# Kernel optimization log

Measured on AMD Instinct MI355X. Metric: run time of the kernel, lower is better.

The kernel has to match this reference:

```python
import jax, jax.numpy as jnp
import numpy as np

B, S, D, H = 2, 2048, 1024, 16
HD = D // H  # head dim = 64


def setup_inputs() -> dict:
    key = jax.random.key(0)
    ks = jax.random.split(key, 8)
    s = 0.02
    return {
        "Q": jax.random.normal(ks[0], (B, S, D), jnp.float32),
        "K": jax.random.normal(ks[1], (B, S, D), jnp.float32),
        "V": jax.random.normal(ks[2], (B, S, D), jnp.float32),
        "mask": jax.random.randint(ks[3], (1, 1, S, S), 0, 2, jnp.int32),
        "Wq": jax.random.normal(ks[4], (D, D), jnp.float32) * s,
        "bq": jnp.zeros((D,), jnp.float32),
        "Wk": jax.random.normal(ks[5], (D, D), jnp.float32) * s,
        "bk": jnp.zeros((D,), jnp.float32),
        "Wv": jax.random.normal(ks[6], (D, D), jnp.float32) * s,
        "bv": jnp.zeros((D,), jnp.float32),
        "Wo": jax.random.normal(ks[7], (D, D), jnp.float32) * s,
        "bo": jnp.zeros((D,), jnp.float32),
    }


def reference(Q, K, V, mask, Wq, bq, Wk, bk, Wv, bv, Wo, bo):
    b = Q.shape[0]
    # QKV projections, split into heads: [B,S,D] -> [B,H,S,HD]
    q = (Q @ Wq + bq).reshape(b, -1, H, HD).transpose(0, 2, 1, 3)
    k = (K @ Wk + bk).reshape(b, -1, H, HD).transpose(0, 2, 1, 3)
    v = (V @ Wv + bv).reshape(b, -1, H, HD).transpose(0, 2, 1, 3)
    # scaled dot-product attention with full [B,H,S,S] scores (as in source)
    scale = jnp.sqrt(jnp.asarray(HD, q.dtype))
    scores = jnp.einsum("bhqd,bhkd->bhqk", q, k) / scale
    scores = jnp.where(mask == 0, -jnp.inf, scores)
    attn = jax.nn.softmax(scores, axis=-1)
    ctx = jnp.einsum("bhqk,bhkd->bhqd", attn, v)
    # merge heads and output projection
    concat = ctx.transpose(0, 2, 1, 3).reshape(b, -1, H * HD)
    return concat @ Wo + bo
```

## Files before the change

kernel.cpp:

```cpp
#include <hip/hip_runtime.h>


using s8v = __attribute__((ext_vector_type(8))) short;
using f4v = __attribute__((ext_vector_type(4))) float;

__device__ __forceinline__ unsigned short f2bf(float f) {
  union { float f; unsigned int u; } v; v.f = f;
  return (unsigned short)((v.u + 0x7fffu + ((v.u >> 16) & 1u)) >> 16);
}

__global__ void f2b3_kernel(const float* __restrict__ A, const float* __restrict__ B,
                            const float* __restrict__ C, unsigned short* __restrict__ oA,
                            unsigned short* __restrict__ oB, unsigned short* __restrict__ oC) {
  int z = blockIdx.x >> 12;
  int idx = (blockIdx.x & 4095) * 256 + threadIdx.x;
  const float* in = (z == 0) ? A : (z == 1) ? B : C;
  unsigned short* out = (z == 0) ? oA : (z == 1) ? oB : oC;
  float4 v = ((const float4*)in)[idx];
  ushort4 o;
  o.x = f2bf(v.x); o.y = f2bf(v.y); o.z = f2bf(v.z); o.w = f2bf(v.w);
  ((ushort4*)out)[idx] = o;
}

__global__ void wtrans4_kernel(const float* __restrict__ W0, const float* __restrict__ W1,
                               const float* __restrict__ W2, const float* __restrict__ W3,
                               unsigned short* __restrict__ T0, unsigned short* __restrict__ T1,
                               unsigned short* __restrict__ T2, unsigned short* __restrict__ T3) {
  __shared__ unsigned short t[64][72];
  int z = blockIdx.z;
  const float* W = (z == 0) ? W0 : (z == 1) ? W1 : (z == 2) ? W2 : W3;
  unsigned short* Wt = (z == 0) ? T0 : (z == 1) ? T1 : (z == 2) ? T2 : T3;
  int k0 = blockIdx.x * 64, n0 = blockIdx.y * 64;
  int tid = threadIdx.x;
  for (int p = 0; p < 4; ++p) {
    int idx = p * 256 + tid;
    int row = idx >> 4;
    int c4  = idx & 15;
    float4 v = *(const float4*)&W[(size_t)(k0 + row) * 1024 + n0 + c4 * 4];
    t[row][c4 * 4 + 0] = f2bf(v.x);
    t[row][c4 * 4 + 1] = f2bf(v.y);
    t[row][c4 * 4 + 2] = f2bf(v.z);
    t[row][c4 * 4 + 3] = f2bf(v.w);
  }
  __syncthreads();
  for (int p = 0; p < 2; ++p) {
    int idx = p * 256 + tid;
    int j  = idx >> 3;
    int c8 = idx & 7;
    unsigned short tmp[8];
    for (int i = 0; i < 8; ++i) tmp[i] = t[c8 * 8 + i][j];
    uint4 o;
    o.x = tmp[0] | ((unsigned)tmp[1] << 16);
    o.y = tmp[2] | ((unsigned)tmp[3] << 16);
    o.z = tmp[4] | ((unsigned)tmp[5] << 16);
    o.w = tmp[6] | ((unsigned)tmp[7] << 16);
    *(uint4*)&Wt[(size_t)(n0 + j) * 1024 + k0 + c8 * 8] = o;
  }
}

__global__ __launch_bounds__(256) void proj3_kernel(
    const unsigned short* __restrict__ A0, const unsigned short* __restrict__ A1,
    const unsigned short* __restrict__ A2,
    const unsigned short* __restrict__ W0, const unsigned short* __restrict__ W1,
    const unsigned short* __restrict__ W2,
    const float* __restrict__ b0, const float* __restrict__ b1, const float* __restrict__ b2,
    unsigned short* __restrict__ oq, unsigned short* __restrict__ ok,
    unsigned short* __restrict__ ovt) {
  const int z = blockIdx.z;
  const unsigned short* A  = (z == 0) ? A0 : (z == 1) ? A1 : A2;
  const unsigned short* Wt = (z == 0) ? W0 : (z == 1) ? W1 : W2;
  const float* bias        = (z == 0) ? b0 : (z == 1) ? b1 : b2;

  __shared__ __align__(16) unsigned short As[128][40];
  __shared__ __align__(16) unsigned short Bs[128][40];

  const int tid = threadIdx.x;
  const int lane = tid & 63, w = tid >> 6, ln = lane & 15, quad = lane >> 4;
  const int wm = (w & 1) * 64, wn = (w >> 1) * 64;
  const int m0 = blockIdx.x * 128, n0 = blockIdx.y * 128;

  f4v zero = {0.f, 0.f, 0.f, 0.f};
  f4v acc[4][4];
  for (int mi = 0; mi < 4; ++mi)
    for (int ni = 0; ni < 4; ++ni) acc[mi][ni] = zero;

  for (int kt = 0; kt < 1024; kt += 32) {
    for (int p = 0; p < 2; ++p) {
      int c = p * 256 + tid;
      int row = c >> 2, c4 = c & 3;
      *(uint4*)&As[row][c4 * 8] = *(const uint4*)&A[(size_t)(m0 + row) * 1024 + kt + c4 * 8];
      *(uint4*)&Bs[row][c4 * 8] = *(const uint4*)&Wt[(size_t)(n0 + row) * 1024 + kt + c4 * 8];
    }
    __syncthreads();
    s8v a[4], b[4];
    for (int mi = 0; mi < 4; ++mi) a[mi] = *(const s8v*)&As[wm + mi * 16 + ln][quad * 8];
    for (int ni = 0; ni < 4; ++ni) b[ni] = *(const s8v*)&Bs[wn + ni * 16 + ln][quad * 8];
    for (int mi = 0; mi < 4; ++mi)
      for (int ni = 0; ni < 4; ++ni)
        acc[mi][ni] = __builtin_amdgcn_mfma_f32_16x16x32_bf16(a[mi], b[ni], acc[mi][ni], 0, 0, 0);
    __syncthreads();
  }

  const float qscale = (z == 0) ? 0.125f : 1.0f;
  if (z < 2) {
    unsigned short* outp = (z == 0) ? oq : ok;
    for (int mi = 0; mi < 4; ++mi) {
      int rb = m0 + wm + mi * 16 + quad * 4;
      int b_ = rb >> 11;
      for (int ni = 0; ni < 4; ++ni) {
        int col = n0 + wn + ni * 16 + ln;
        float bvv = bias[col];
        int h = col >> 6, hd = col & 63;
        size_t ob = (size_t)(b_ * 16 + h) * 2048;
        for (int r = 0; r < 4; ++r) {
          int s = (rb + r) & 2047;
          outp[(ob + s) * 64 + hd] = f2bf((acc[mi][ni][r] + bvv) * qscale);
        }
      }
    }
  } else {
    for (int mi = 0; mi < 4; ++mi) {
      int rb = m0 + wm + mi * 16 + quad * 4;
      int b_ = rb >> 11, s = rb & 2047;
      for (int ni = 0; ni < 4; ++ni) {
        int col = n0 + wn + ni * 16 + ln;
        float bvv = bias[col];
        int h = col >> 6, hd = col & 63;
        ushort4 o;
        o.x = f2bf(acc[mi][ni][0] + bvv);
        o.y = f2bf(acc[mi][ni][1] + bvv);
        o.z = f2bf(acc[mi][ni][2] + bvv);
        o.w = f2bf(acc[mi][ni][3] + bvv);
        *(ushort4*)&ovt[((size_t)(b_ * 16 + h) * 64 + hd) * 2048 + s] = o;
      }
    }
  }
}

__global__ __launch_bounds__(256) void flash_kernel(
    const unsigned short* __restrict__ q, const unsigned short* __restrict__ k,
    const unsigned short* __restrict__ vt, const int* __restrict__ mask,
    unsigned short* __restrict__ ctx) {
  __shared__ __align__(16) unsigned short qp_s[64][72];
  __shared__ __align__(16) unsigned short k_s[64][72];
  __shared__ __align__(16) unsigned short v_s[64][72];

  const int tid = threadIdx.x;
  const int lane = tid & 63, w = tid >> 6, ln = lane & 15, quad = lane >> 4;
  const int q0 = blockIdx.x * 64;
  const int bh = blockIdx.y;
  const unsigned short* qg  = q  + ((size_t)bh * 2048 + q0) * 64;
  const unsigned short* kgb = k  + (size_t)bh * 2048 * 64;
  const unsigned short* vgb = vt + (size_t)bh * 64 * 2048;

  for (int p = 0; p < 2; ++p) {
    int c = p * 256 + tid;
    int row = c >> 3, c8 = c & 7;
    *(uint4*)&qp_s[row][c8 * 8] = *(const uint4*)&qg[(size_t)row * 64 + c8 * 8];
  }
  __syncthreads();
  s8v aq[2];
  aq[0] = *(const s8v*)&qp_s[w * 16 + ln][quad * 8];
  aq[1] = *(const s8v*)&qp_s[w * 16 + ln][32 + quad * 8];

  const int srow0 = tid >> 3, sc8 = tid & 7;
  const int srow1 = 32 + srow0;

  uint4 kr0 = *(const uint4*)&kgb[(size_t)srow0 * 64 + sc8 * 8];
  uint4 kr1 = *(const uint4*)&kgb[(size_t)srow1 * 64 + sc8 * 8];
  uint4 vr0 = *(const uint4*)&vgb[(size_t)srow0 * 2048 + sc8 * 8];
  uint4 vr1 = *(const uint4*)&vgb[(size_t)srow1 * 2048 + sc8 * 8];

  f4v zero = {0.f, 0.f, 0.f, 0.f};
  float lsum[4] = {0.f, 0.f, 0.f, 0.f};
  f4v o_acc[4];
  for (int ni = 0; ni < 4; ++ni) o_acc[ni] = zero;

  for (int kt = 0; kt < 2048; kt += 64) {
    *(uint4*)&k_s[srow0][sc8 * 8] = kr0;
    *(uint4*)&k_s[srow1][sc8 * 8] = kr1;
    *(uint4*)&v_s[srow0][sc8 * 8] = vr0;
    *(uint4*)&v_s[srow1][sc8 * 8] = vr1;
    if (kt + 64 < 2048) {
      kr0 = *(const uint4*)&kgb[(size_t)(kt + 64 + srow0) * 64 + sc8 * 8];
      kr1 = *(const uint4*)&kgb[(size_t)(kt + 64 + srow1) * 64 + sc8 * 8];
      vr0 = *(const uint4*)&vgb[(size_t)srow0 * 2048 + kt + 64 + sc8 * 8];
      vr1 = *(const uint4*)&vgb[(size_t)srow1 * 2048 + kt + 64 + sc8 * 8];
    }
    __syncthreads();

    f4v sc[4];
    for (int ni = 0; ni < 4; ++ni) {
      sc[ni] = zero;
      s8v bk0 = *(const s8v*)&k_s[ni * 16 + ln][quad * 8];
      s8v bk1 = *(const s8v*)&k_s[ni * 16 + ln][32 + quad * 8];
      sc[ni] = __builtin_amdgcn_mfma_f32_16x16x32_bf16(aq[0], bk0, sc[ni], 0, 0, 0);
      sc[ni] = __builtin_amdgcn_mfma_f32_16x16x32_bf16(aq[1], bk1, sc[ni], 0, 0, 0);
    }

    const int rg0 = q0 + w * 16 + quad * 4;
    for (int ni = 0; ni < 4; ++ni) {
      int colg = kt + ni * 16 + ln;
      const int* mrow = &mask[(size_t)rg0 * 2048 + colg];
      for (int r = 0; r < 4; ++r) {
        int mv = mrow[r * 2048];
        float e = mv ? __expf(sc[ni][r]) : 0.f;
        unsigned int u = __float_as_uint(e);
        lsum[r] += __uint_as_float(u & 0xffff0000u);
        qp_s[w * 16 + quad * 4 + r][ni * 16 + ln] = (unsigned short)(u >> 16);
      }
    }

    s8v ap0 = *(const s8v*)&qp_s[w * 16 + ln][quad * 8];
    s8v ap1 = *(const s8v*)&qp_s[w * 16 + ln][32 + quad * 8];
    for (int ni = 0; ni < 4; ++ni) {
      s8v bv0 = *(const s8v*)&v_s[ni * 16 + ln][quad * 8];
      s8v bv1 = *(const s8v*)&v_s[ni * 16 + ln][32 + quad * 8];
      o_acc[ni] = __builtin_amdgcn_mfma_f32_16x16x32_bf16(ap0, bv0, o_acc[ni], 0, 0, 0);
      o_acc[ni] = __builtin_amdgcn_mfma_f32_16x16x32_bf16(ap1, bv1, o_acc[ni], 0, 0, 0);
    }
    __syncthreads();
  }

  int b_ = bh >> 4, h = bh & 15;
  for (int r = 0; r < 4; ++r) {
    float l = lsum[r];
    for (int off = 1; off < 16; off <<= 1) l += __shfl_xor(l, off);
    float inv = 1.f / l;
    int srow = q0 + w * 16 + quad * 4 + r;
    size_t base = ((size_t)b_ * 2048 + srow) * 1024 + h * 64;
    for (int ni = 0; ni < 4; ++ni)
      ctx[base + ni * 16 + ln] = f2bf(o_acc[ni][r] * inv);
  }
}

__global__ __launch_bounds__(256) void gemm_out_kernel(
    const unsigned short* __restrict__ A, const unsigned short* __restrict__ Wt,
    const float* __restrict__ bias, float* __restrict__ out) {
  __shared__ __align__(16) unsigned short As[128][40];
  __shared__ __align__(16) unsigned short Bs[128][40];

  const int tid = threadIdx.x;
  const int lane = tid & 63, w = tid >> 6, ln = lane & 15, quad = lane >> 4;
  const int wm = (w & 1) * 64, wn = (w >> 1) * 64;
  const int m0 = blockIdx.x * 128, n0 = blockIdx.y * 128;

  f4v zero = {0.f, 0.f, 0.f, 0.f};
  f4v acc[4][4];
  for (int mi = 0; mi < 4; ++mi)
    for (int ni = 0; ni < 4; ++ni) acc[mi][ni] = zero;

  for (int kt = 0; kt < 1024; kt += 32) {
    for (int p = 0; p < 2; ++p) {
      int c = p * 256 + tid;
      int row = c >> 2, c4 = c & 3;
      *(uint4*)&As[row][c4 * 8] = *(const uint4*)&A[(size_t)(m0 + row) * 1024 + kt + c4 * 8];
      *(uint4*)&Bs[row][c4 * 8] = *(const uint4*)&Wt[(size_t)(n0 + row) * 1024 + kt + c4 * 8];
    }
    __syncthreads();
    s8v a[4], b[4];
    for (int mi = 0; mi < 4; ++mi) a[mi] = *(const s8v*)&As[wm + mi * 16 + ln][quad * 8];
    for (int ni = 0; ni < 4; ++ni) b[ni] = *(const s8v*)&Bs[wn + ni * 16 + ln][quad * 8];
    for (int mi = 0; mi < 4; ++mi)
      for (int ni = 0; ni < 4; ++ni)
        acc[mi][ni] = __builtin_amdgcn_mfma_f32_16x16x32_bf16(a[mi], b[ni], acc[mi][ni], 0, 0, 0);
    __syncthreads();
  }

  for (int mi = 0; mi < 4; ++mi) {
    int rb = m0 + wm + mi * 16 + quad * 4;
    for (int ni = 0; ni < 4; ++ni) {
      int col = n0 + wn + ni * 16 + ln;
      float bvv = bias[col];
      for (int r = 0; r < 4; ++r)
        out[(size_t)(rb + r) * 1024 + col] = acc[mi][ni][r] + bvv;
    }
  }
}

extern "C" void kernel_launch(void* const* d_in, const int* in_sizes, int n_in,
                              void* d_out, int out_size, void* d_ws, size_t ws_size,
                              hipStream_t stream) {
  const float* Q  = (const float*)d_in[0];
  const float* K  = (const float*)d_in[1];
  const float* V  = (const float*)d_in[2];
  const int* mask = (const int*)d_in[3];
  const float* Wq = (const float*)d_in[4];
  const float* bq = (const float*)d_in[5];
  const float* Wk = (const float*)d_in[6];
  const float* bk = (const float*)d_in[7];
  const float* Wv = (const float*)d_in[8];
  const float* bv = (const float*)d_in[9];
  const float* Wo = (const float*)d_in[10];
  const float* bo = (const float*)d_in[11];
  float* out = (float*)d_out;

  char* ws = (char*)d_ws;
  const size_t MB = 1u << 20;
  unsigned short* qb  = (unsigned short*)(ws + 0 * MB);
  unsigned short* kb  = (unsigned short*)(ws + 8 * MB);
  unsigned short* vb  = (unsigned short*)(ws + 16 * MB);
  unsigned short* wqt = (unsigned short*)(ws + 24 * MB);
  unsigned short* wkt = (unsigned short*)(ws + 26 * MB);
  unsigned short* wvt = (unsigned short*)(ws + 28 * MB);
  unsigned short* wot = (unsigned short*)(ws + 30 * MB);
  unsigned short* qh  = (unsigned short*)(ws + 32 * MB);
  unsigned short* kh  = (unsigned short*)(ws + 40 * MB);
  unsigned short* vth = (unsigned short*)(ws + 48 * MB);
  unsigned short* ctx = (unsigned short*)(ws + 56 * MB);

  f2b3_kernel<<<12288, 256, 0, stream>>>(Q, K, V, qb, kb, vb);
  wtrans4_kernel<<<dim3(16, 16, 4), 256, 0, stream>>>(Wq, Wk, Wv, Wo, wqt, wkt, wvt, wot);
  proj3_kernel<<<dim3(32, 8, 3), 256, 0, stream>>>(qb, kb, vb, wqt, wkt, wvt,
                                                   bq, bk, bv, qh, kh, vth);
  flash_kernel<<<dim3(32, 32), 256, 0, stream>>>(qh, kh, vth, mask, ctx);
  gemm_out_kernel<<<dim3(32, 8), 256, 0, stream>>>(ctx, wot, bo, out);
}
```

Baseline: 279.5 us.

## Pack attention mask to bits, prefetch GEMM tiles in registers, use exp2

Adds a kernel that packs the int32 mask into 64-bit ballot words. The flash kernel then reads one word per row per key tile, prefetched a tile ahead, instead of many scattered int loads, and it applies the mask by multiplying with a 0/1 float. The Q scale now folds in log2(e) so the kernel can call the hardware exp2. Both GEMM kernels also prefetch the next K-slice into registers while the current one is computed. The packed mask reuses the workspace region of the bf16 Q copy, which is safe only because projection has already consumed it. The extra kernel launch adds some overhead.

```diff
diff --git a/kernel.cpp b/kernel.cpp
--- a/kernel.cpp
+++ b/kernel.cpp
@@ -3,6 +3,7 @@
 
 using s8v = __attribute__((ext_vector_type(8))) short;
 using f4v = __attribute__((ext_vector_type(4))) float;
+typedef unsigned long long u64;
 
 __device__ __forceinline__ unsigned short f2bf(float f) {
   union { float f; unsigned int u; } v; v.f = f;
@@ -20,6 +21,14 @@
   ushort4 o;
   o.x = f2bf(v.x); o.y = f2bf(v.y); o.z = f2bf(v.z); o.w = f2bf(v.w);
   ((ushort4*)out)[idx] = o;
+}
+
+__global__ void packmask_kernel(const int* __restrict__ mask, u64* __restrict__ bm) {
+  int gw = (int)((blockIdx.x * 256 + threadIdx.x) >> 6);
+  int lane = threadIdx.x & 63;
+  int mv = mask[(size_t)gw * 64 + lane];
+  u64 bal = __ballot(mv != 0);
+  if (lane == 0) bm[gw] = bal;
 }
 
 __global__ void wtrans4_kernel(const float* __restrict__ W0, const float* __restrict__ W1,
@@ -79,17 +88,29 @@
   const int wm = (w & 1) * 64, wn = (w >> 1) * 64;
   const int m0 = blockIdx.x * 128, n0 = blockIdx.y * 128;
 
+  const int r0 = tid >> 2, c40 = tid & 3;
+  const int r1 = (tid + 256) >> 2, c41 = tid & 3;
+
+  uint4 ar0 = *(const uint4*)&A[(size_t)(m0 + r0) * 1024 + c40 * 8];
+  uint4 ar1 = *(const uint4*)&A[(size_t)(m0 + r1) * 1024 + c41 * 8];
+  uint4 br0 = *(const uint4*)&Wt[(size_t)(n0 + r0) * 1024 + c40 * 8];
+  uint4 br1 = *(const uint4*)&Wt[(size_t)(n0 + r1) * 1024 + c41 * 8];
+
   f4v zero = {0.f, 0.f, 0.f, 0.f};
   f4v acc[4][4];
   for (int mi = 0; mi < 4; ++mi)
     for (int ni = 0; ni < 4; ++ni) acc[mi][ni] = zero;
 
   for (int kt = 0; kt < 1024; kt += 32) {
-    for (int p = 0; p < 2; ++p) {
-      int c = p * 256 + tid;
-      int row = c >> 2, c4 = c & 3;
-      *(uint4*)&As[row][c4 * 8] = *(const uint4*)&A[(size_t)(m0 + row) * 1024 + kt + c4 * 8];
-      *(uint4*)&Bs[row][c4 * 8] = *(const uint4*)&Wt[(size_t)(n0 + row) * 1024 + kt + c4 * 8];
+    *(uint4*)&As[r0][c40 * 8] = ar0;
+    *(uint4*)&As[r1][c41 * 8] = ar1;
+    *(uint4*)&Bs[r0][c40 * 8] = br0;
+    *(uint4*)&Bs[r1][c41 * 8] = br1;
+    if (kt + 32 < 1024) {
+      ar0 = *(const uint4*)&A[(size_t)(m0 + r0) * 1024 + kt + 32 + c40 * 8];
+      ar1 = *(const uint4*)&A[(size_t)(m0 + r1) * 1024 + kt + 32 + c41 * 8];
+      br0 = *(const uint4*)&Wt[(size_t)(n0 + r0) * 1024 + kt + 32 + c40 * 8];
+      br1 = *(const uint4*)&Wt[(size_t)(n0 + r1) * 1024 + kt + 32 + c41 * 8];
     }
     __syncthreads();
     s8v a[4], b[4];
@@ -101,7 +122,7 @@
     __syncthreads();
   }
 
-  const float qscale = (z == 0) ? 0.125f : 1.0f;
+  const float qscale = (z == 0) ? 0.18033688f : 1.0f;
   if (z < 2) {
     unsigned short* outp = (z == 0) ? oq : ok;
     for (int mi = 0; mi < 4; ++mi) {
@@ -139,7 +160,7 @@
 
 __global__ __launch_bounds__(256) void flash_kernel(
     const unsigned short* __restrict__ q, const unsigned short* __restrict__ k,
-    const unsigned short* __restrict__ vt, const int* __restrict__ mask,
+    const unsigned short* __restrict__ vt, const u64* __restrict__ bm,
     unsigned short* __restrict__ ctx) {
   __shared__ __align__(16) unsigned short qp_s[64][72];
   __shared__ __align__(16) unsigned short k_s[64][72];
@@ -152,6 +173,7 @@
   const unsigned short* qg  = q  + ((size_t)bh * 2048 + q0) * 64;
   const unsigned short* kgb = k  + (size_t)bh * 2048 * 64;
   const unsigned short* vgb = vt + (size_t)bh * 64 * 2048;
+  const u64* bmr = bm + (size_t)(q0 + w * 16 + quad * 4) * 32;
 
   for (int p = 0; p < 2; ++p) {
     int c = p * 256 + tid;
@@ -170,6 +192,8 @@
   uint4 kr1 = *(const uint4*)&kgb[(size_t)srow1 * 64 + sc8 * 8];
   uint4 vr0 = *(const uint4*)&vgb[(size_t)srow0 * 2048 + sc8 * 8];
   uint4 vr1 = *(const uint4*)&vgb[(size_t)srow1 * 2048 + sc8 * 8];
+  u64 mwc[4], mwn[4];
+  for (int r = 0; r < 4; ++r) mwc[r] = bmr[r * 32];
 
   f4v zero = {0.f, 0.f, 0.f, 0.f};
   float lsum[4] = {0.f, 0.f, 0.f, 0.f};
@@ -182,10 +206,13 @@
     *(uint4*)&v_s[srow0][sc8 * 8] = vr0;
     *(uint4*)&v_s[srow1][sc8 * 8] = vr1;
     if (kt + 64 < 2048) {
-      kr0 = *(const uint4*)&kgb[(size_t)(kt + 64 + srow0) * 64 + sc8 * 8];
-      kr1 = *(const uint4*)&kgb[(size_t)(kt + 64 + srow1) * 64 + sc8 * 8];
-      vr0 = *(const uint4*)&vgb[(size_t)srow0 * 2048 + kt + 64 + sc8 * 8];
-      vr1 = *(const uint4*)&vgb[(size_t)srow1 * 2048 + kt + 64 + sc8 * 8];
+      int ktn = kt + 64;
+      kr0 = *(const uint4*)&kgb[(size_t)(ktn + srow0) * 64 + sc8 * 8];
+      kr1 = *(const uint4*)&kgb[(size_t)(ktn + srow1) * 64 + sc8 * 8];
+      vr0 = *(const uint4*)&vgb[(size_t)srow0 * 2048 + ktn + sc8 * 8];
+      vr1 = *(const uint4*)&vgb[(size_t)srow1 * 2048 + ktn + sc8 * 8];
+      int ktcn = ktn >> 6;
+      for (int r = 0; r < 4; ++r) mwn[r] = bmr[r * 32 + ktcn];
     }
     __syncthreads();
 
@@ -198,18 +225,22 @@
       sc[ni] = __builtin_amdgcn_mfma_f32_16x16x32_bf16(aq[1], bk1, sc[ni], 0, 0, 0);
     }
 
-    const int rg0 = q0 + w * 16 + quad * 4;
-    for (int ni = 0; ni < 4; ++ni) {
-      int colg = kt + ni * 16 + ln;
-      const int* mrow = &mask[(size_t)rg0 * 2048 + colg];
-      for (int r = 0; r < 4; ++r) {
-        int mv = mrow[r * 2048];
-        float e = mv ? __expf(sc[ni][r]) : 0.f;
+    for (int r = 0; r < 4; ++r) {
+      u64 m = mwc[r] >> ln;
+      unsigned mlo = (unsigned)m, mhi = (unsigned)(m >> 32);
+      float f[4];
+      f[0] = (float)(mlo & 1u);
+      f[1] = (float)((mlo >> 16) & 1u);
+      f[2] = (float)(mhi & 1u);
+      f[3] = (float)((mhi >> 16) & 1u);
+      for (int ni = 0; ni < 4; ++ni) {
+        float e = __builtin_amdgcn_exp2f(sc[ni][r]) * f[ni];
         unsigned int u = __float_as_uint(e);
         lsum[r] += __uint_as_float(u & 0xffff0000u);
         qp_s[w * 16 + quad * 4 + r][ni * 16 + ln] = (unsigned short)(u >> 16);
       }
     }
+    for (int r = 0; r < 4; ++r) mwc[r] = mwn[r];
 
     s8v ap0 = *(const s8v*)&qp_s[w * 16 + ln][quad * 8];
     s8v ap1 = *(const s8v*)&qp_s[w * 16 + ln][32 + quad * 8];
@@ -245,17 +276,29 @@
   const int wm = (w & 1) * 64, wn = (w >> 1) * 64;
   const int m0 = blockIdx.x * 128, n0 = blockIdx.y * 128;
 
+  const int r0 = tid >> 2, c40 = tid & 3;
+  const int r1 = (tid + 256) >> 2, c41 = tid & 3;
+
+  uint4 ar0 = *(const uint4*)&A[(size_t)(m0 + r0) * 1024 + c40 * 8];
+  uint4 ar1 = *(const uint4*)&A[(size_t)(m0 + r1) * 1024 + c41 * 8];
+  uint4 br0 = *(const uint4*)&Wt[(size_t)(n0 + r0) * 1024 + c40 * 8];
+  uint4 br1 = *(const uint4*)&Wt[(size_t)(n0 + r1) * 1024 + c41 * 8];
+
   f4v zero = {0.f, 0.f, 0.f, 0.f};
   f4v acc[4][4];
   for (int mi = 0; mi < 4; ++mi)
     for (int ni = 0; ni < 4; ++ni) acc[mi][ni] = zero;
 
   for (int kt = 0; kt < 1024; kt += 32) {
-    for (int p = 0; p < 2; ++p) {
-      int c = p * 256 + tid;
-      int row = c >> 2, c4 = c & 3;
-      *(uint4*)&As[row][c4 * 8] = *(const uint4*)&A[(size_t)(m0 + row) * 1024 + kt + c4 * 8];
-      *(uint4*)&Bs[row][c4 * 8] = *(const uint4*)&Wt[(size_t)(n0 + row) * 1024 + kt + c4 * 8];
+    *(uint4*)&As[r0][c40 * 8] = ar0;
+    *(uint4*)&As[r1][c41 * 8] = ar1;
+    *(uint4*)&Bs[r0][c40 * 8] = br0;
+    *(uint4*)&Bs[r1][c41 * 8] = br1;
+    if (kt + 32 < 1024) {
+      ar0 = *(const uint4*)&A[(size_t)(m0 + r0) * 1024 + kt + 32 + c40 * 8];
+      ar1 = *(const uint4*)&A[(size_t)(m0 + r1) * 1024 + kt + 32 + c41 * 8];
+      br0 = *(const uint4*)&Wt[(size_t)(n0 + r0) * 1024 + kt + 32 + c40 * 8];
+      br1 = *(const uint4*)&Wt[(size_t)(n0 + r1) * 1024 + kt + 32 + c41 * 8];
     }
     __syncthreads();
     s8v a[4], b[4];
@@ -308,11 +351,13 @@
   unsigned short* kh  = (unsigned short*)(ws + 40 * MB);
   unsigned short* vth = (unsigned short*)(ws + 48 * MB);
   unsigned short* ctx = (unsigned short*)(ws + 56 * MB);
+  u64* bm = (u64*)(ws + 0 * MB);
 
   f2b3_kernel<<<12288, 256, 0, stream>>>(Q, K, V, qb, kb, vb);
   wtrans4_kernel<<<dim3(16, 16, 4), 256, 0, stream>>>(Wq, Wk, Wv, Wo, wqt, wkt, wvt, wot);
   proj3_kernel<<<dim3(32, 8, 3), 256, 0, stream>>>(qb, kb, vb, wqt, wkt, wvt,
                                                    bq, bk, bv, qh, kh, vth);
-  flash_kernel<<<dim3(32, 32), 256, 0, stream>>>(qh, kh, vth, mask, ctx);
+  packmask_kernel<<<16384, 256, 0, stream>>>(mask, bm);
+  flash_kernel<<<dim3(32, 32), 256, 0, stream>>>(qh, kh, vth, bm, ctx);
   gemm_out_kernel<<<dim3(32, 8), 256, 0, stream>>>(ctx, wot, bo, out);
 }
```

After: 276.8 us. No clear change (-0.9%).
